# Performance work log

Hardware: AMD Instinct MI355X
Metric: run time of the kernel (lower is better)

## Reference

```python
import jax, jax.numpy as jnp
import numpy as np

EPS = 1e-08
SURROGATE_SCALE = 10.0  # SuperSpike surrogate slope

@jax.custom_vjp
def spike_fn(v):
    # Heaviside forward, SuperSpike surrogate gradient backward
    return (v > 0).astype(v.dtype)

def _spike_fwd(v):
    return spike_fn(v), v

def _spike_bwd(v, g):
    return (g / (1.0 + SURROGATE_SCALE * jnp.abs(v)) ** 2,)

spike_fn.defvjp(_spike_fwd, _spike_bwd)


def setup_inputs() -> dict:
    key = jax.random.key(0)
    k1, k2, k3, k4 = jax.random.split(key, 4)
    B, C, T = 64, 256, 2048
    x = jax.random.normal(k1, (B, C, T), dtype=jnp.float32)
    conv_weight = jax.random.normal(k2, (C, C, 3), dtype=jnp.float32) * 0.05
    beta = jnp.clip(0.7 + 0.01 * jax.random.normal(k3, (1,), dtype=jnp.float32), 0.0, 1.0)
    b = jnp.clip(1.0 + 0.01 * jax.random.normal(k4, (C,), dtype=jnp.float32), 0.0, None)
    return {"x": x, "conv_weight": conv_weight, "beta": beta, "b": b}


def reference(x, conv_weight, beta, b):
    # x: (B, C, T); LIF recurrence over T with scaled threshold/reset
    norm = (conv_weight ** 2).sum((1, 2))          # (C,)
    inv_norm = 1.0 / (norm + EPS)                   # (C,)
    B, C, T = x.shape
    xt = jnp.transpose(x, (2, 0, 1))                # (T, B, C)

    def step(carry, inp):
        mem, spk = carry
        rst = spk * (b * norm)                      # einsum ab,b,b->ab
        mem = (mem - rst) * beta + inp * (1.0 - beta)
        mthr = mem * inv_norm - b
        spk = spike_fn(mthr)
        return (mem, spk), spk

    init = (jnp.zeros((B, C), x.dtype), jnp.zeros((B, C), x.dtype))
    _, spk_rec = jax.lax.scan(step, init, xt)       # (T, B, C)
    return jnp.transpose(spk_rec, (1, 2, 0))        # (B, C, T), flatten_output=False
```

## Files before the change

### kernel.cpp

```cpp
#include <hip/hip_runtime.h>

#define C_DIM 256
#define T_DIM 2048
#define B_DIM 64
#define NROWS (B_DIM * C_DIM)
#define SEGS 8
#define SEGL (T_DIM / SEGS)
#define WARM 128
#define PW   64
#define NPH  ((WARM + SEGL) / PW)
#define WARM_PH (WARM / PW)
#define SPITCH 68
#define NSTR 64

__device__ __forceinline__ float sqrn(float v) { return __fmul_rn(v, v); }

__global__ __launch_bounds__(64) void norm_kernel(const float* __restrict__ w,
                                                  const float* __restrict__ b,
                                                  float* __restrict__ bn,
                                                  float* __restrict__ ninv) {
    const int c = blockIdx.x;
    const int k = threadIdx.x;
    __shared__ float q[8];
    if (k < 8) {
        const float* a = w + c * 768 + k * 96;
        float r0 = sqrn(a[0]), r1 = sqrn(a[1]), r2 = sqrn(a[2]), r3 = sqrn(a[3]);
        float r4 = sqrn(a[4]), r5 = sqrn(a[5]), r6 = sqrn(a[6]), r7 = sqrn(a[7]);
        #pragma unroll
        for (int i = 8; i < 96; i += 8) {
            r0 = __fadd_rn(r0, sqrn(a[i + 0]));
            r1 = __fadd_rn(r1, sqrn(a[i + 1]));
            r2 = __fadd_rn(r2, sqrn(a[i + 2]));
            r3 = __fadd_rn(r3, sqrn(a[i + 3]));
            r4 = __fadd_rn(r4, sqrn(a[i + 4]));
            r5 = __fadd_rn(r5, sqrn(a[i + 5]));
            r6 = __fadd_rn(r6, sqrn(a[i + 6]));
            r7 = __fadd_rn(r7, sqrn(a[i + 7]));
        }
        q[k] = __fadd_rn(__fadd_rn(__fadd_rn(r0, r1), __fadd_rn(r2, r3)),
                         __fadd_rn(__fadd_rn(r4, r5), __fadd_rn(r6, r7)));
    }
    __syncthreads();
    if (k == 0) {
        float s = __fadd_rn(__fadd_rn(__fadd_rn(q[0], q[1]), __fadd_rn(q[2], q[3])),
                            __fadd_rn(__fadd_rn(q[4], q[5]), __fadd_rn(q[6], q[7])));
        bn[c]   = __fmul_rn(b[c], s);
        ninv[c] = 1.0f / __fadd_rn(s, 1e-8f);
    }
}

__device__ __forceinline__ float step_fast(float xw, float& mem, int& mask,
                                           float bnc, float beta, float nic, float bc) {
    float m0 = __fmul_rn(mem, beta);
    float m1 = __fmul_rn(__fsub_rn(mem, bnc), beta);
    m0 = __fadd_rn(m0, xw);
    m1 = __fadd_rn(m1, xw);
    int mi = (__float_as_int(m1) & mask) | (__float_as_int(m0) & ~mask);
    mem = __int_as_float(mi);
    float p = __fmul_rn(mem, nic);
    float d = __fsub_rn(bc, p);
    mask = __float_as_int(d) >> 31;
    return __int_as_float(mask & 0x3f800000);
}

#define STEP4_NOSTORE(v)                                                   \
    do {                                                                   \
        float xw0 = __fmul_rn((v).x, omb);                                 \
        float xw1 = __fmul_rn((v).y, omb);                                 \
        float xw2 = __fmul_rn((v).z, omb);                                 \
        float xw3 = __fmul_rn((v).w, omb);                                 \
        (void)step_fast(xw0, mem, mask, bnc, beta, nic, bc);               \
        (void)step_fast(xw1, mem, mask, bnc, beta, nic, bc);               \
        (void)step_fast(xw2, mem, mask, bnc, beta, nic, bc);               \
        (void)step_fast(xw3, mem, mask, bnc, beta, nic, bc);               \
    } while (0)

#define STEP4_STORE(v, o)                                                  \
    do {                                                                   \
        float xw0 = __fmul_rn((v).x, omb);                                 \
        float xw1 = __fmul_rn((v).y, omb);                                 \
        float xw2 = __fmul_rn((v).z, omb);                                 \
        float xw3 = __fmul_rn((v).w, omb);                                 \
        (o).x = step_fast(xw0, mem, mask, bnc, beta, nic, bc);             \
        (o).y = step_fast(xw1, mem, mask, bnc, beta, nic, bc);             \
        (o).z = step_fast(xw2, mem, mask, bnc, beta, nic, bc);             \
        (o).w = step_fast(xw3, mem, mask, bnc, beta, nic, bc);             \
    } while (0)

#define WAITCNT_LGKM0  0xC07F

__global__ __launch_bounds__(64) void lif_seg_kernel(const float* __restrict__ x,
                                                     const float* __restrict__ beta_p,
                                                     const float* __restrict__ b,
                                                     const float* __restrict__ bn,
                                                     const float* __restrict__ ninv,
                                                     float* __restrict__ out) {
    __shared__ __align__(16) float lds[NSTR * SPITCH];

    const int lane = threadIdx.x;
    const int seg  = lane & 7;
    const int row  = blockIdx.x * 8 + (lane >> 3);
    const int c    = row & (C_DIM - 1);

    const float beta = beta_p[0];
    const float omb  = __fsub_rn(1.0f, beta);
    const float bnc  = bn[c];
    const float nic  = ninv[c];
    const float bc   = b[c];

    const int fh = lane >> 4;
    const int fj = lane & 15;

    float mem = 0.0f;
    int   mask = 0;

    float* my = &lds[lane * SPITCH];

    #pragma unroll 1
    for (int P = 0; P < NPH; ++P) {
        #pragma unroll
        for (int q = 0; q < 16; ++q) {
            const int s    = 4 * q + fh;
            const int srow = blockIdx.x * 8 + (s >> 3);
            int rel = (s & 7) * SEGL - WARM + P * PW;
            if (rel < 0) rel = 0;
            const float* g = x + (size_t)srow * T_DIM + rel + 4 * fj;
            float4 v = *(const float4*)g;
            *(float4*)(&lds[s * SPITCH + 4 * fj]) = v;
        }
        __builtin_amdgcn_s_waitcnt(WAITCNT_LGKM0);

        if (P < WARM_PH) {
            #pragma unroll
            for (int g = 0; g < PW / 4; ++g) {
                float4 v = *(const float4*)(my + 4 * g);
                STEP4_NOSTORE(v);
            }
            if (P == WARM_PH - 1) {
                if (seg == 0) { mem = 0.0f; mask = 0; }
            }
        } else {
            #pragma unroll
            for (int g = 0; g < PW / 4; ++g) {
                float4 v = *(const float4*)(my + 4 * g);
                float4 o;
                STEP4_STORE(v, o);
                *(float4*)(my + 4 * g) = o;
            }
            __builtin_amdgcn_s_waitcnt(WAITCNT_LGKM0);

            #pragma unroll
            for (int q = 0; q < 16; ++q) {
                const int s    = 4 * q + fh;
                const int srow = blockIdx.x * 8 + (s >> 3);
                const int rel  = (s & 7) * SEGL - WARM + P * PW;
                float4 v = *(const float4*)(&lds[s * SPITCH + 4 * fj]);
                *(float4*)(out + (size_t)srow * T_DIM + rel + 4 * fj) = v;
            }
        }
    }
}

extern "C" void kernel_launch(void* const* d_in, const int* in_sizes, int n_in,
                              void* d_out, int out_size, void* d_ws, size_t ws_size,
                              hipStream_t stream) {
    const float* x    = (const float*)d_in[0];
    const float* w    = (const float*)d_in[1];
    const float* beta = (const float*)d_in[2];
    const float* b    = (const float*)d_in[3];
    float* out  = (float*)d_out;
    float* bn   = (float*)d_ws;
    float* ninv = bn + C_DIM;

    norm_kernel<<<C_DIM, 64, 0, stream>>>(w, b, bn, ninv);
    lif_seg_kernel<<<(NROWS * SEGS) / NSTR, NSTR, 0, stream>>>(x, beta, b, bn, ninv, out);
}
```

Measured before the change: 252.9 us.

## Double-buffer input tiles with async global_load_lds and swizzled LDS layout

Replaces the synchronous global-to-register-to-LDS copy with asynchronous global_load_lds transfers into two LDS buffers. The next phase's chunk is prefetched while the current one is processed. The phase width shrinks from 64 to 32 so both buffers fit. The padded pitch gives way to a rotated per-segment swizzle, which avoids bank conflicts and matches the direct-to-LDS lane mapping. The aim is to hide global load latency behind the serial LIF recurrence, at the cost of more phases and hand-tuned vmcnt waits that must correctly account for the interleaved stores.

```diff
diff --git a/kernel.cpp b/kernel.cpp
--- a/kernel.cpp
+++ b/kernel.cpp
@@ -7,10 +7,9 @@
 #define SEGS 8
 #define SEGL (T_DIM / SEGS)
 #define WARM 128
-#define PW   64
+#define PW   32
 #define NPH  ((WARM + SEGL) / PW)
 #define WARM_PH (WARM / PW)
-#define SPITCH 68
 #define NSTR 64
 
 __device__ __forceinline__ float sqrn(float v) { return __fmul_rn(v, v); }
@@ -87,7 +86,12 @@
         (o).w = step_fast(xw3, mem, mask, bnc, beta, nic, bc);             \
     } while (0)
 
+#define WAITCNT_VM0    0x0F70
+#define WAITCNT_VM8    0x0F78
 #define WAITCNT_LGKM0  0xC07F
+
+#define LDS_PTR(p) ((__attribute__((address_space(3))) void*)(p))
+#define GLB_PTR(p) ((const __attribute__((address_space(1))) void*)(p))
 
 __global__ __launch_bounds__(64) void lif_seg_kernel(const float* __restrict__ x,
                                                      const float* __restrict__ beta_p,
@@ -95,11 +99,12 @@
                                                      const float* __restrict__ bn,
                                                      const float* __restrict__ ninv,
                                                      float* __restrict__ out) {
-    __shared__ __align__(16) float lds[NSTR * SPITCH];
+    __shared__ __align__(16) float lds[2][NSTR * PW];
 
     const int lane = threadIdx.x;
     const int seg  = lane & 7;
-    const int row  = blockIdx.x * 8 + (lane >> 3);
+    const int row0 = blockIdx.x * 8;
+    const int row  = row0 + (lane >> 3);
     const int c    = row & (C_DIM - 1);
 
     const float beta = beta_p[0];
@@ -108,54 +113,64 @@
     const float nic  = ninv[c];
     const float bc   = b[c];
 
-    const int fh = lane >> 4;
-    const int fj = lane & 15;
+    const int fseg = lane >> 3;
+    const int fg   = ((lane & 7) - fseg) & 7;
 
     float mem = 0.0f;
     int   mask = 0;
 
-    float* my = &lds[lane * SPITCH];
+    {
+        int rel = fseg * SEGL - WARM;
+        if (rel < 0) rel = 0;
+        #pragma unroll
+        for (int q = 0; q < 8; ++q) {
+            const float* g = x + (size_t)(row0 + q) * T_DIM + rel + 4 * fg;
+            __builtin_amdgcn_global_load_lds(GLB_PTR(g), LDS_PTR(&lds[0][q * 256]), 16, 0, 0);
+        }
+    }
 
     #pragma unroll 1
     for (int P = 0; P < NPH; ++P) {
-        #pragma unroll
-        for (int q = 0; q < 16; ++q) {
-            const int s    = 4 * q + fh;
-            const int srow = blockIdx.x * 8 + (s >> 3);
-            int rel = (s & 7) * SEGL - WARM + P * PW;
-            if (rel < 0) rel = 0;
-            const float* g = x + (size_t)srow * T_DIM + rel + 4 * fj;
-            float4 v = *(const float4*)g;
-            *(float4*)(&lds[s * SPITCH + 4 * fj]) = v;
+        if (P >= 5) __builtin_amdgcn_s_waitcnt(WAITCNT_VM8);
+        else        __builtin_amdgcn_s_waitcnt(WAITCNT_VM0);
+
+        if (P + 1 < NPH) {
+            int relb = fseg * SEGL - WARM + (P + 1) * PW;
+            if (relb < 0) relb = 0;
+            float* dbuf = &lds[(P + 1) & 1][0];
+            #pragma unroll
+            for (int q = 0; q < 8; ++q) {
+                const float* g = x + (size_t)(row0 + q) * T_DIM + relb + 4 * fg;
+                __builtin_amdgcn_global_load_lds(GLB_PTR(g), LDS_PTR(dbuf + q * 256), 16, 0, 0);
+            }
         }
-        __builtin_amdgcn_s_waitcnt(WAITCNT_LGKM0);
+
+        float* buf = &lds[P & 1][0];
+        float* my  = buf + lane * PW;
 
         if (P < WARM_PH) {
             #pragma unroll
             for (int g = 0; g < PW / 4; ++g) {
-                float4 v = *(const float4*)(my + 4 * g);
+                float4 v = *(const float4*)(my + 4 * ((g + seg) & 7));
                 STEP4_NOSTORE(v);
             }
-            if (P == WARM_PH - 1) {
-                if (seg == 0) { mem = 0.0f; mask = 0; }
-            }
+            if (P == WARM_PH - 1 && seg == 0) { mem = 0.0f; mask = 0; }
         } else {
             #pragma unroll
             for (int g = 0; g < PW / 4; ++g) {
-                float4 v = *(const float4*)(my + 4 * g);
+                float* p = my + 4 * ((g + seg) & 7);
+                float4 v = *(const float4*)p;
                 float4 o;
                 STEP4_STORE(v, o);
-                *(float4*)(my + 4 * g) = o;
+                *(float4*)p = o;
             }
             __builtin_amdgcn_s_waitcnt(WAITCNT_LGKM0);
 
+            const size_t ob = (size_t)fseg * SEGL + (size_t)(P * PW - WARM) + 4 * fg;
             #pragma unroll
-            for (int q = 0; q < 16; ++q) {
-                const int s    = 4 * q + fh;
-                const int srow = blockIdx.x * 8 + (s >> 3);
-                const int rel  = (s & 7) * SEGL - WARM + P * PW;
-                float4 v = *(const float4*)(&lds[s * SPITCH + 4 * fj]);
-                *(float4*)(out + (size_t)srow * T_DIM + rel + 4 * fj) = v;
+            for (int q = 0; q < 8; ++q) {
+                float4 v = *(const float4*)(buf + q * 256 + 4 * lane);
+                *(float4*)(out + (size_t)(row0 + q) * T_DIM + ob) = v;
             }
         }
     }
```

Result: no change. 256.6 us (+1.5%).
